# Kernel tuning notes

Measured on AMD Instinct MI355X. Metric: run time of the kernel, lower is better.

## Reference

```python
import jax, jax.numpy as jnp
import numpy as np

ROT_DIM = 32  # min(32, dim_head)

def rotate_half(t):
    # '... (j d) -> ... j d' with j=2, unbind, cat(-x2, x1)
    x1, x2 = jnp.split(t, 2, axis=-1)
    return jnp.concatenate((-x2, x1), axis=-1)

def apply_rotary(pos, t):
    rot_dim = pos.shape[-1]
    t_rot, t_pass = t[..., :rot_dim], t[..., rot_dim:]
    t_rot = t_rot * jnp.cos(pos) + rotate_half(t_rot) * jnp.sin(pos)
    return jnp.concatenate((t_rot, t_pass), axis=-1)

def setup_inputs() -> dict:
    key = jax.random.key(0)
    k1, k2, k3 = jax.random.split(key, 3)
    b, n, dim = 2, 2048, 2048
    inner = 16 * 128
    x = jax.random.normal(k1, (b, n, dim), dtype=jnp.float32)
    w_qkv = jax.random.normal(k2, (3 * inner, dim), dtype=jnp.float32) * (dim ** -0.5)
    w_out = jax.random.normal(k3, (inner, dim), dtype=jnp.float32) * (inner ** -0.5)
    g = jnp.ones((dim,), dtype=jnp.float32)
    return {"x": x, "w_qkv": w_qkv, "w_out": w_out, "g": g}

def reference(x, w_qkv, w_out, g):
    b, n, dim = x.shape
    h, d = 16, 128
    scale = d ** -0.5
    # NOTE: original code computes qkv from RAW x; the LayerNorm result is unused.
    qkv = jnp.einsum('bnc,fc->bnf', x, w_qkv)  # [b, n, 3*h*d]
    q, k, v = jnp.split(qkv, 3, axis=-1)
    def to_heads(t):  # b n (h d) -> (b h) n d
        return t.reshape(b, n, h, d).transpose(0, 2, 1, 3).reshape(b * h, n, d)
    q, k, v = map(to_heads, (q, k, v))
    # rotary positions: freqs [n, ROT_DIM//2], cat -> [n, ROT_DIM]
    inv_freq = 1.0 / (10000.0 ** (jnp.arange(0, ROT_DIM, 2, dtype=jnp.float32) / ROT_DIM))
    freqs = jnp.arange(n, dtype=jnp.float32)[:, None] * inv_freq[None, :]
    pos = jnp.concatenate((freqs, freqs), axis=-1)  # [n, ROT_DIM]
    q = apply_rotary(pos, q)
    k = apply_rotary(pos, k)
    q = q * scale
    sim = jnp.einsum('bid,bjd->bij', q, k)  # [(b h), n, n]
    causal_mask = jnp.triu(jnp.ones((n, n), dtype=bool), 1)
    neg = -jnp.finfo(sim.dtype).max
    sim = jnp.where(causal_mask[None], neg, sim)
    attn = jax.nn.softmax(sim, axis=-1)
    out = jnp.einsum('bij,bjd->bid', attn, v)  # [(b h), n, d]
    out = out.reshape(b, h, n, d).transpose(0, 2, 1, 3).reshape(b, n, h * d)
    return jnp.einsum('bnf,fc->bnc', out, w_out.T)  # Linear(inner, dim): y = out @ w_out^T with w_out [inner, dim]? see note
```

## Files before the change

### kernel.cpp

```cpp
#include <hip/hip_runtime.h>
#include <hip/hip_bf16.h>
#include <stdint.h>

typedef __bf16 bf16_t;
typedef __bf16 bf16x8 __attribute__((ext_vector_type(8)));
typedef float  f32x4  __attribute__((ext_vector_type(4)));

__device__ __forceinline__ void gload16(const void* gp, void* lp) {
  __builtin_amdgcn_global_load_lds(
      (const __attribute__((address_space(1))) void*)(uintptr_t)gp,
      (__attribute__((address_space(3))) void*)(uintptr_t)lp,
      16, 0, 0);
}

__device__ __forceinline__ f32x4 mfma16(bf16x8 a, bf16x8 b, f32x4 c) {
  return __builtin_amdgcn_mfma_f32_16x16x32_bf16(a, b, c, 0, 0, 0);
}

__device__ __forceinline__ uint32_t pack2(float a, float b) {
  uint16_t ba = __builtin_bit_cast(uint16_t, (bf16_t)a);
  uint16_t bb = __builtin_bit_cast(uint16_t, (bf16_t)b);
  return (uint32_t)ba | ((uint32_t)bb << 16);
}

__global__ __launch_bounds__(256) void cast_f32_to_bf16(const float* __restrict__ in,
                                                        bf16_t* __restrict__ out, int n8) {
  int i = blockIdx.x * 256 + threadIdx.x;
  int stride = gridDim.x * 256;
  for (; i < n8; i += stride) {
    const f32x4* p = (const f32x4*)in + (size_t)i * 2;
    f32x4 a = p[0], b = p[1];
    bf16x8 o;
    o[0] = (bf16_t)a[0]; o[1] = (bf16_t)a[1]; o[2] = (bf16_t)a[2]; o[3] = (bf16_t)a[3];
    o[4] = (bf16_t)b[0]; o[5] = (bf16_t)b[1]; o[6] = (bf16_t)b[2]; o[7] = (bf16_t)b[3];
    ((bf16x8*)out)[i] = o;
  }
}

template<bool OUT_BF16>
__global__ __launch_bounds__(512, 2) void gemm_bt_wide(const bf16_t* __restrict__ A,
                                                       const bf16_t* __restrict__ B,
                                                       void* __restrict__ Cout,
                                                       int M, int N, int K) {
  __shared__ __align__(16) bf16_t As[2][256 * 64];
  __shared__ __align__(16) bf16_t Bs[2][192 * 64];
  const int t = threadIdx.x;
  const int wid = t >> 6, l = t & 63;
  const int l15 = l & 15, l4 = l >> 4;
  const int wm = wid >> 1, wn = wid & 1;
  const long m0 = (long)blockIdx.x * 256;
  const long n0 = (long)blockIdx.y * 192;
  const int KT = K >> 6;

  auto stageA = [&](int kt, bf16_t* __restrict__ LB) {
    #pragma unroll
    for (int it = 0; it < 4; ++it) {
      int s = it * 512 + t;
      int r = s >> 3, c = s & 7;
      gload16(A + (m0 + r) * (long)K + kt * 64 + ((c ^ (r & 7)) << 3),
              LB + r * 64 + c * 8);
    }
  };
  auto stageB = [&](int kt, bf16_t* __restrict__ LB) {
    #pragma unroll
    for (int it = 0; it < 3; ++it) {
      int s = it * 512 + t;
      int r = s >> 3, c = s & 7;
      gload16(B + (n0 + r) * (long)K + kt * 64 + ((c ^ (r & 7)) << 3),
              LB + r * 64 + c * 8);
    }
  };
  auto ldfrag = [&](const bf16_t* buf, int rloc, int kk) -> bf16x8 {
    return *(const bf16x8*)(buf + rloc * 64 + ((((kk << 2) + l4) ^ (rloc & 7)) << 3));
  };

  f32x4 acc[4][6] = {};

  stageB(0, &Bs[0][0]);
  stageA(0, &As[0][0]);
  stageB(1, &Bs[1][0]);
  asm volatile("s_waitcnt vmcnt(3)" ::: "memory");
  asm volatile("s_barrier" ::: "memory");

  for (int kt = 0; kt < KT; ++kt) {
    const bf16_t* Ab = &As[kt & 1][0];
    const bf16_t* Bb = &Bs[kt & 1][0];
    const bool stA = (kt + 1 < KT), stB = (kt + 2 < KT);

    bf16x8 bfr[6][2];
    #pragma unroll
    for (int nr = 0; nr < 6; ++nr)
      #pragma unroll
      for (int kk = 0; kk < 2; ++kk)
        bfr[nr][kk] = ldfrag(Bb, wn * 96 + nr * 16 + l15, kk);
    {
      bf16x8 a0 = ldfrag(Ab, wm * 64 + 0 * 16 + l15, 0);
      bf16x8 a1 = ldfrag(Ab, wm * 64 + 1 * 16 + l15, 0);
      bf16x8 a2 = ldfrag(Ab, wm * 64 + 2 * 16 + l15, 0);
      bf16x8 a3 = ldfrag(Ab, wm * 64 + 3 * 16 + l15, 0);
      if (stA) stageA(kt + 1, &As[(kt + 1) & 1][0]);
      asm volatile("s_barrier" ::: "memory");
      asm volatile("s_waitcnt lgkmcnt(0)" ::: "memory");
      __builtin_amdgcn_sched_barrier(0);
      __builtin_amdgcn_s_setprio(1);
      #pragma unroll
      for (int nr = 0; nr < 6; ++nr) {
        acc[0][nr] = mfma16(a0, bfr[nr][0], acc[0][nr]);
        acc[1][nr] = mfma16(a1, bfr[nr][0], acc[1][nr]);
        acc[2][nr] = mfma16(a2, bfr[nr][0], acc[2][nr]);
        acc[3][nr] = mfma16(a3, bfr[nr][0], acc[3][nr]);
      }
      __builtin_amdgcn_s_setprio(0);
      asm volatile("s_barrier" ::: "memory");
    }
    {
      bf16x8 a0 = ldfrag(Ab, wm * 64 + 0 * 16 + l15, 1);
      bf16x8 a1 = ldfrag(Ab, wm * 64 + 1 * 16 + l15, 1);
      bf16x8 a2 = ldfrag(Ab, wm * 64 + 2 * 16 + l15, 1);
      bf16x8 a3 = ldfrag(Ab, wm * 64 + 3 * 16 + l15, 1);
      if (stB) stageB(kt + 2, &Bs[kt & 1][0]);
      asm volatile("s_barrier" ::: "memory");
      asm volatile("s_waitcnt lgkmcnt(0)" ::: "memory");
      __builtin_amdgcn_sched_barrier(0);
      __builtin_amdgcn_s_setprio(1);
      #pragma unroll
      for (int nr = 0; nr < 6; ++nr) {
        acc[0][nr] = mfma16(a0, bfr[nr][1], acc[0][nr]);
        acc[1][nr] = mfma16(a1, bfr[nr][1], acc[1][nr]);
        acc[2][nr] = mfma16(a2, bfr[nr][1], acc[2][nr]);
        acc[3][nr] = mfma16(a3, bfr[nr][1], acc[3][nr]);
      }
      __builtin_amdgcn_s_setprio(0);
      if (stB) asm volatile("s_waitcnt vmcnt(3)" ::: "memory");
      else     asm volatile("s_waitcnt vmcnt(0)" ::: "memory");
      asm volatile("s_barrier" ::: "memory");
    }
  }

  #pragma unroll
  for (int mr = 0; mr < 4; ++mr)
    #pragma unroll
    for (int nr = 0; nr < 6; ++nr)
      #pragma unroll
      for (int i = 0; i < 4; ++i) {
        long r = m0 + wm * 64 + mr * 16 + l4 * 4 + i;
        long c = n0 + wn * 96 + nr * 16 + l15;
        if (OUT_BF16) ((bf16_t*)Cout)[r * N + c] = (bf16_t)acc[mr][nr][i];
        else          ((float*)Cout)[r * N + c] = acc[mr][nr][i];
      }
}

template<bool OUT_BF16>
__global__ __launch_bounds__(512, 2) void gemm8p_bt(const bf16_t* __restrict__ A,
                                                    const bf16_t* __restrict__ B,
                                                    void* __restrict__ Cout,
                                                    int M, int N, int K) {
  __shared__ __align__(16) bf16_t As[2][128 * 64];
  __shared__ __align__(16) bf16_t Bs[2][256 * 64];
  const int t = threadIdx.x;
  const int wid = t >> 6, l = t & 63;
  const int l15 = l & 15, l4 = l >> 4;
  const int wm = wid >> 2, wn = wid & 3;
  const long m0 = (long)blockIdx.x * 128;
  const long n0 = (long)blockIdx.y * 256;
  const int KT = K >> 6;

  auto stageA = [&](int kt, bf16_t* __restrict__ LB) {
    #pragma unroll
    for (int it = 0; it < 2; ++it) {
      int s = it * 512 + t;
      int r = s >> 3, c = s & 7;
      gload16(A + (m0 + r) * (long)K + kt * 64 + ((c ^ (r & 7)) << 3),
              LB + r * 64 + c * 8);
    }
  };
  auto stageB = [&](int kt, bf16_t* __restrict__ LB) {
    #pragma unroll
    for (int it = 0; it < 4; ++it) {
      int s = it * 512 + t;
      int r = s >> 3, c = s & 7;
      gload16(B + (n0 + r) * (long)K + kt * 64 + ((c ^ (r & 7)) << 3),
              LB + r * 64 + c * 8);
    }
  };
  auto ldfrag = [&](const bf16_t* buf, int rloc, int kk) -> bf16x8 {
    return *(const bf16x8*)(buf + rloc * 64 + ((((kk << 2) + l4) ^ (rloc & 7)) << 3));
  };

  f32x4 acc[4][4] = {};

  stageB(0, &Bs[0][0]);
  stageA(0, &As[0][0]);
  stageB(1, &Bs[1][0]);
  asm volatile("s_waitcnt vmcnt(4)" ::: "memory");
  asm volatile("s_barrier" ::: "memory");

  for (int kt = 0; kt < KT; ++kt) {
    const bf16_t* Ab = &As[kt & 1][0];
    const bf16_t* Bb = &Bs[kt & 1][0];
    const bool stA = (kt + 1 < KT), stB = (kt + 2 < KT);

    bf16x8 bfr[4][2];
    #pragma unroll
    for (int nr = 0; nr < 4; ++nr)
      #pragma unroll
      for (int kk = 0; kk < 2; ++kk)
        bfr[nr][kk] = ldfrag(Bb, wn * 64 + nr * 16 + l15, kk);
    {
      bf16x8 a00 = ldfrag(Ab, wm * 64 + 0 * 16 + l15, 0);
      bf16x8 a01 = ldfrag(Ab, wm * 64 + 0 * 16 + l15, 1);
      bf16x8 a10 = ldfrag(Ab, wm * 64 + 1 * 16 + l15, 0);
      bf16x8 a11 = ldfrag(Ab, wm * 64 + 1 * 16 + l15, 1);
      if (stA) stageA(kt + 1, &As[(kt + 1) & 1][0]);
      asm volatile("s_barrier" ::: "memory");
      asm volatile("s_waitcnt lgkmcnt(0)" ::: "memory");
      __builtin_amdgcn_sched_barrier(0);
      __builtin_amdgcn_s_setprio(1);
      #pragma unroll
      for (int nr = 0; nr < 4; ++nr) {
        acc[0][nr] = mfma16(a00, bfr[nr][0], acc[0][nr]);
        acc[0][nr] = mfma16(a01, bfr[nr][1], acc[0][nr]);
        acc[1][nr] = mfma16(a10, bfr[nr][0], acc[1][nr]);
        acc[1][nr] = mfma16(a11, bfr[nr][1], acc[1][nr]);
      }
      __builtin_amdgcn_s_setprio(0);
      asm volatile("s_barrier" ::: "memory");
    }
    {
      bf16x8 a00 = ldfrag(Ab, wm * 64 + 2 * 16 + l15, 0);
      bf16x8 a01 = ldfrag(Ab, wm * 64 + 2 * 16 + l15, 1);
      bf16x8 a10 = ldfrag(Ab, wm * 64 + 3 * 16 + l15, 0);
      bf16x8 a11 = ldfrag(Ab, wm * 64 + 3 * 16 + l15, 1);
      if (stB) stageB(kt + 2, &Bs[kt & 1][0]);
      asm volatile("s_barrier" ::: "memory");
      asm volatile("s_waitcnt lgkmcnt(0)" ::: "memory");
      __builtin_amdgcn_sched_barrier(0);
      __builtin_amdgcn_s_setprio(1);
      #pragma unroll
      for (int nr = 0; nr < 4; ++nr) {
        acc[2][nr] = mfma16(a00, bfr[nr][0], acc[2][nr]);
        acc[2][nr] = mfma16(a01, bfr[nr][1], acc[2][nr]);
        acc[3][nr] = mfma16(a10, bfr[nr][0], acc[3][nr]);
        acc[3][nr] = mfma16(a11, bfr[nr][1], acc[3][nr]);
      }
      __builtin_amdgcn_s_setprio(0);
      if (stB) asm volatile("s_waitcnt vmcnt(4)" ::: "memory");
      else     asm volatile("s_waitcnt vmcnt(0)" ::: "memory");
      asm volatile("s_barrier" ::: "memory");
    }
  }

  #pragma unroll
  for (int mr = 0; mr < 4; ++mr)
    #pragma unroll
    for (int nr = 0; nr < 4; ++nr)
      #pragma unroll
      for (int i = 0; i < 4; ++i) {
        long r = m0 + wm * 64 + mr * 16 + l4 * 4 + i;
        long c = n0 + wn * 64 + nr * 16 + l15;
        if (OUT_BF16) ((bf16_t*)Cout)[r * N + c] = (bf16_t)acc[mr][nr][i];
        else          ((float*)Cout)[r * N + c] = acc[mr][nr][i];
      }
}

__global__ __launch_bounds__(256) void rope_scale(bf16_t* __restrict__ qkv) {
  int t = blockIdx.x * 256 + threadIdx.x;
  int m = t >> 8;
  int h = (t >> 4) & 15;
  int j = t & 15;
  int n = m & 2047;
  const float L2_10000_D16 = 0.8304820237218406f;
  float inv = exp2f(-(float)j * L2_10000_D16);
  float ang = (float)n * inv;
  float s, c;
  sincosf(ang, &s, &c);
  const float scale = 0.08838834764831845f;
  bf16_t* qp = qkv + (long)m * 6144 + h * 128;
  float a = (float)qp[j], b = (float)qp[j + 16];
  qp[j]      = (bf16_t)((a * c - b * s) * scale);
  qp[j + 16] = (bf16_t)((b * c + a * s) * scale);
  #pragma unroll
  for (int u = 0; u < 6; ++u) {
    int d = 32 + j + u * 16;
    qp[d] = (bf16_t)((float)qp[d] * scale);
  }
  bf16_t* kp = qp + 2048;
  a = (float)kp[j]; b = (float)kp[j + 16];
  kp[j]      = (bf16_t)(a * c - b * s);
  kp[j + 16] = (bf16_t)(b * c + a * s);
}

__global__ __launch_bounds__(512, 4) void attn_causal(const bf16_t* __restrict__ qkv,
                                                      bf16_t* __restrict__ ao) {
  const int id = blockIdx.x;
  const int qt = 15 - (id >> 5);
  const int bh = id & 31;
  const int b = bh >> 4, h = bh & 15;
  const int t = threadIdx.x;
  const int wid = t >> 6, l = t & 63;
  const int l15 = l & 15, l4 = l >> 4;
  __shared__ __align__(16) bf16_t Ks0[64 * 128];
  __shared__ __align__(16) bf16_t Ks1[64 * 128];
  __shared__ __align__(16) bf16_t Vt[128 * 64];
  __shared__ __align__(16) bf16_t Pb[8][16 * 72];
  const bf16_t* base = qkv + (long)b * 2048 * 6144 + h * 128;
  const int q0w = qt * 128 + wid * 16;
  bf16x8 qf[4];
  #pragma unroll
  for (int ks = 0; ks < 4; ++ks)
    qf[ks] = *(const bf16x8*)(base + (long)(q0w + l15) * 6144 + ks * 32 + l4 * 8);
  f32x4 o[8] = {};
  float mrun = -1.0e30f, lrun = 0.f;
  bf16_t* pbuf = Pb[wid];
  bf16x8 vr0, vr1;
  const int ntiles = 2 * qt + 2;

  auto stageK = [&](int tile, bf16_t* dst) {
    const bf16_t* src = base + 2048 + (long)tile * 64 * 6144;
    #pragma unroll
    for (int it = 0; it < 2; ++it) {
      int s = it * 512 + t;
      int krow = s >> 4, kc = s & 15;
      int ksc = kc ^ (krow & 7);
      gload16(src + (long)krow * 6144 + ksc * 8, dst + (size_t)s * 8);
    }
  };
  auto loadV = [&](int tile) {
    const bf16_t* vsr = base + 4096 + (long)(tile * 64 + l) * 6144;
    vr0 = *(const bf16x8*)(vsr + wid * 8);
    vr1 = *(const bf16x8*)(vsr + (8 + wid) * 8);
  };
  auto writeVt = [&]() {
    #pragma unroll
    for (int it = 0; it < 2; ++it) {
      int c = it * 8 + wid;
      bf16x8 v = it ? vr1 : vr0;
      #pragma unroll
      for (int e = 0; e < 8; ++e) {
        int d = c * 8 + e;
        Vt[d * 64 + (((l >> 3) ^ e) * 8) + (l & 7)] = v[e];
      }
    }
  };
  auto compute = [&](int kv0, const bf16_t* ksb) {
    if (kv0 > q0w + 15) return;
    f32x4 sa[4] = {};
    __builtin_amdgcn_s_setprio(1);
    #pragma unroll
    for (int ks = 0; ks < 4; ++ks) {
      #pragma unroll
      for (int nb = 0; nb < 4; ++nb) {
        int row = nb * 16 + l15;
        int cs = (ks * 4 + l4) ^ (row & 7);
        bf16x8 kf = *(const bf16x8*)(ksb + row * 128 + cs * 8);
        sa[nb] = mfma16(kf, qf[ks], sa[nb]);
      }
    }
    __builtin_amdgcn_s_setprio(0);
    if (kv0 + 63 > q0w) {
      const int q = q0w + l15;
      #pragma unroll
      for (int nb = 0; nb < 4; ++nb)
        #pragma unroll
        for (int i = 0; i < 4; ++i)
          if (kv0 + nb * 16 + l4 * 4 + i > q) sa[nb][i] = -3.0e38f;
    }
    f32x4 mv;
    #pragma unroll
    for (int i = 0; i < 4; ++i)
      mv[i] = fmaxf(fmaxf(sa[0][i], sa[1][i]), fmaxf(sa[2][i], sa[3][i]));
    float pmax = fmaxf(fmaxf(mv[0], mv[1]), fmaxf(mv[2], mv[3]));
    pmax = fmaxf(pmax, __shfl_xor(pmax, 16));
    pmax = fmaxf(pmax, __shfl_xor(pmax, 32));
    if (!__all(pmax - mrun <= 8.0f)) {
      float mnew = fmaxf(mrun, pmax);
      float corr = __expf(mrun - mnew);
      mrun = mnew;
      lrun *= corr;
      float cc[4];
      #pragma unroll
      for (int i = 0; i < 4; ++i) cc[i] = __shfl(corr, l4 * 4 + i);
      #pragma unroll
      for (int nf = 0; nf < 8; ++nf)
        #pragma unroll
        for (int i = 0; i < 4; ++i) o[nf][i] *= cc[i];
    }
    float ps = 0.f;
    #pragma unroll
    for (int nb = 0; nb < 4; ++nb)
      #pragma unroll
      for (int i = 0; i < 4; ++i) {
        float p = __expf(sa[nb][i] - mrun);
        sa[nb][i] = p;
        ps += p;
      }
    ps += __shfl_xor(ps, 16);
    ps += __shfl_xor(ps, 32);
    lrun += ps;
    #pragma unroll
    for (int nb = 0; nb < 4; ++nb) {
      int cw = (nb * 2 + (l4 >> 1)) ^ (l15 & 7);
      uint32_t* dst = (uint32_t*)(pbuf + l15 * 72 + cw * 8 + (l4 & 1) * 4);
      dst[0] = pack2(sa[nb][0], sa[nb][1]);
      dst[1] = pack2(sa[nb][2], sa[nb][3]);
    }
    #pragma unroll
    for (int ks2 = 0; ks2 < 2; ++ks2) {
      bf16x8 pf = *(const bf16x8*)(pbuf + l15 * 72 + (((ks2 * 4 + l4) ^ (l15 & 7)) * 8));
      __builtin_amdgcn_s_setprio(1);
      #pragma unroll
      for (int nf = 0; nf < 8; ++nf) {
        int row = nf * 16 + l15;
        bf16x8 vf = *(const bf16x8*)(Vt + row * 64 + (((ks2 * 4 + l4) ^ (row & 7)) * 8));
        o[nf] = mfma16(pf, vf, o[nf]);
      }
      __builtin_amdgcn_s_setprio(0);
    }
  };

  stageK(0, Ks0);
  loadV(0);
  writeVt();
  __syncthreads();
  for (int tile = 0; tile < ntiles; ++tile) {
    bf16_t* cur = (tile & 1) ? Ks1 : Ks0;
    bf16_t* nxt = (tile & 1) ? Ks0 : Ks1;
    const bool pre = (tile + 1 < ntiles);
    if (pre) { stageK(tile + 1, nxt); loadV(tile + 1); }
    compute(tile * 64, cur);
    __syncthreads();
    if (pre) writeVt();
    __syncthreads();
  }
  float linv = 1.f / lrun;
  float li[4];
  #pragma unroll
  for (int i = 0; i < 4; ++i) li[i] = __shfl(linv, l4 * 4 + i);
  bf16_t* aob = ao + (long)b * 2048 * 2048 + h * 128;
  #pragma unroll
  for (int i = 0; i < 4; ++i) {
    long qrow = q0w + l4 * 4 + i;
    #pragma unroll
    for (int nf = 0; nf < 8; ++nf)
      aob[qrow * 2048 + nf * 16 + l15] = (bf16_t)(o[nf][i] * li[i]);
  }
}

extern "C" void kernel_launch(void* const* d_in, const int* in_sizes, int n_in,
                              void* d_out, int out_size, void* d_ws, size_t ws_size,
                              hipStream_t stream) {
  const float* x     = (const float*)d_in[0];
  const float* w_qkv = (const float*)d_in[1];
  const float* w_out = (const float*)d_in[2];
  char* ws = (char*)d_ws;
  bf16_t* xb    = (bf16_t*)(ws + 0L);
  bf16_t* wqkvb = (bf16_t*)(ws + 16777216L);
  bf16_t* woutb = (bf16_t*)(ws + 41943040L);
  bf16_t* qkv   = (bf16_t*)(ws + 50331648L);
  bf16_t* ao    = (bf16_t*)(ws + 100663296L);

  cast_f32_to_bf16<<<2048, 256, 0, stream>>>(x, xb, 1048576);
  cast_f32_to_bf16<<<2048, 256, 0, stream>>>(w_qkv, wqkvb, 1572864);
  cast_f32_to_bf16<<<1024, 256, 0, stream>>>(w_out, woutb, 524288);
  gemm_bt_wide<true ><<<dim3(16, 32), 512, 0, stream>>>(xb, wqkvb, (void*)qkv, 4096, 6144, 2048);
  rope_scale<<<4096, 256, 0, stream>>>(qkv);
  attn_causal<<<512, 512, 0, stream>>>(qkv, ao);
  gemm8p_bt<false><<<dim3(32, 8), 512, 0, stream>>>(ao, woutb, d_out, 4096, 2048, 2048);
}
```

Before: 260.1 us.

## Widen QKV GEMM tile to 256x384 with K-step 32 and 8x6 accumulators

```diff
diff --git a/kernel.cpp b/kernel.cpp
--- a/kernel.cpp
+++ b/kernel.cpp
@@ -37,44 +37,41 @@
   }
 }
 
-template<bool OUT_BF16>
-__global__ __launch_bounds__(512, 2) void gemm_bt_wide(const bf16_t* __restrict__ A,
-                                                       const bf16_t* __restrict__ B,
-                                                       void* __restrict__ Cout,
-                                                       int M, int N, int K) {
-  __shared__ __align__(16) bf16_t As[2][256 * 64];
-  __shared__ __align__(16) bf16_t Bs[2][192 * 64];
+__global__ __launch_bounds__(512, 2) void gemm_qkv(const bf16_t* __restrict__ A,
+                                                   const bf16_t* __restrict__ B,
+                                                   bf16_t* __restrict__ C,
+                                                   int M, int N, int K) {
+  __shared__ __align__(16) bf16_t As[2][256 * 32];
+  __shared__ __align__(16) bf16_t Bs[2][384 * 32];
   const int t = threadIdx.x;
   const int wid = t >> 6, l = t & 63;
   const int l15 = l & 15, l4 = l >> 4;
-  const int wm = wid >> 1, wn = wid & 1;
+  const int wm = wid >> 2, wn = wid & 3;
   const long m0 = (long)blockIdx.x * 256;
-  const long n0 = (long)blockIdx.y * 192;
-  const int KT = K >> 6;
+  const long n0 = (long)blockIdx.y * 384;
+  const int KT = K >> 5;
 
   auto stageA = [&](int kt, bf16_t* __restrict__ LB) {
     #pragma unroll
-    for (int it = 0; it < 4; ++it) {
+    for (int it = 0; it < 2; ++it) {
       int s = it * 512 + t;
-      int r = s >> 3, c = s & 7;
-      gload16(A + (m0 + r) * (long)K + kt * 64 + ((c ^ (r & 7)) << 3),
-              LB + r * 64 + c * 8);
+      int r = s >> 2, c = s & 3;
+      gload16(A + (m0 + r) * (long)K + kt * 32 + c * 8, LB + r * 32 + c * 8);
     }
   };
   auto stageB = [&](int kt, bf16_t* __restrict__ LB) {
     #pragma unroll
     for (int it = 0; it < 3; ++it) {
       int s = it * 512 + t;
-      int r = s >> 3, c = s & 7;
-      gload16(B + (n0 + r) * (long)K + kt * 64 + ((c ^ (r & 7)) << 3),
-              LB + r * 64 + c * 8);
-    }
-  };
-  auto ldfrag = [&](const bf16_t* buf, int rloc, int kk) -> bf16x8 {
-    return *(const bf16x8*)(buf + rloc * 64 + ((((kk << 2) + l4) ^ (rloc & 7)) << 3));
-  };
-
-  f32x4 acc[4][6] = {};
+      int r = s >> 2, c = s & 3;
+      gload16(B + (n0 + r) * (long)K + kt * 32 + c * 8, LB + r * 32 + c * 8);
+    }
+  };
+  auto ldfrag = [&](const bf16_t* buf, int rloc) -> bf16x8 {
+    return *(const bf16x8*)(buf + rloc * 32 + l4 * 8);
+  };
+
+  f32x4 acc[8][6] = {};
 
   stageB(0, &Bs[0][0]);
   stageA(0, &As[0][0]);
@@ -87,17 +84,14 @@
     const bf16_t* Bb = &Bs[kt & 1][0];
     const bool stA = (kt + 1 < KT), stB = (kt + 2 < KT);
 
-    bf16x8 bfr[6][2];
-    #pragma unroll
-    for (int nr = 0; nr < 6; ++nr)
-      #pragma unroll
-      for (int kk = 0; kk < 2; ++kk)
-        bfr[nr][kk] = ldfrag(Bb, wn * 96 + nr * 16 + l15, kk);
+    bf16x8 bfr[6];
+    #pragma unroll
+    for (int nr = 0; nr < 6; ++nr) bfr[nr] = ldfrag(Bb, wn * 96 + nr * 16 + l15);
     {
-      bf16x8 a0 = ldfrag(Ab, wm * 64 + 0 * 16 + l15, 0);
-      bf16x8 a1 = ldfrag(Ab, wm * 64 + 1 * 16 + l15, 0);
-      bf16x8 a2 = ldfrag(Ab, wm * 64 + 2 * 16 + l15, 0);
-      bf16x8 a3 = ldfrag(Ab, wm * 64 + 3 * 16 + l15, 0);
+      bf16x8 a0 = ldfrag(Ab, wm * 128 + 0 * 16 + l15);
+      bf16x8 a1 = ldfrag(Ab, wm * 128 + 1 * 16 + l15);
+      bf16x8 a2 = ldfrag(Ab, wm * 128 + 2 * 16 + l15);
+      bf16x8 a3 = ldfrag(Ab, wm * 128 + 3 * 16 + l15);
       if (stA) stageA(kt + 1, &As[(kt + 1) & 1][0]);
       asm volatile("s_barrier" ::: "memory");
       asm volatile("s_waitcnt lgkmcnt(0)" ::: "memory");
@@ -105,19 +99,19 @@
       __builtin_amdgcn_s_setprio(1);
       #pragma unroll
       for (int nr = 0; nr < 6; ++nr) {
-        acc[0][nr] = mfma16(a0, bfr[nr][0], acc[0][nr]);
-        acc[1][nr] = mfma16(a1, bfr[nr][0], acc[1][nr]);
-        acc[2][nr] = mfma16(a2, bfr[nr][0], acc[2][nr]);
-        acc[3][nr] = mfma16(a3, bfr[nr][0], acc[3][nr]);
+        acc[0][nr] = mfma16(a0, bfr[nr], acc[0][nr]);
+        acc[1][nr] = mfma16(a1, bfr[nr], acc[1][nr]);
+        acc[2][nr] = mfma16(a2, bfr[nr], acc[2][nr]);
+        acc[3][nr] = mfma16(a3, bfr[nr], acc[3][nr]);
       }
       __builtin_amdgcn_s_setprio(0);
       asm volatile("s_barrier" ::: "memory");
     }
     {
-      bf16x8 a0 = ldfrag(Ab, wm * 64 + 0 * 16 + l15, 1);
-      bf16x8 a1 = ldfrag(Ab, wm * 64 + 1 * 16 + l15, 1);
-      bf16x8 a2 = ldfrag(Ab, wm * 64 + 2 * 16 + l15, 1);
-      bf16x8 a3 = ldfrag(Ab, wm * 64 + 3 * 16 + l15, 1);
+      bf16x8 a4 = ldfrag(Ab, wm * 128 + 4 * 16 + l15);
+      bf16x8 a5 = ldfrag(Ab, wm * 128 + 5 * 16 + l15);
+      bf16x8 a6 = ldfrag(Ab, wm * 128 + 6 * 16 + l15);
+      bf16x8 a7 = ldfrag(Ab, wm * 128 + 7 * 16 + l15);
       if (stB) stageB(kt + 2, &Bs[kt & 1][0]);
       asm volatile("s_barrier" ::: "memory");
       asm volatile("s_waitcnt lgkmcnt(0)" ::: "memory");
@@ -125,10 +119,10 @@
       __builtin_amdgcn_s_setprio(1);
       #pragma unroll
       for (int nr = 0; nr < 6; ++nr) {
-        acc[0][nr] = mfma16(a0, bfr[nr][1], acc[0][nr]);
-        acc[1][nr] = mfma16(a1, bfr[nr][1], acc[1][nr]);
-        acc[2][nr] = mfma16(a2, bfr[nr][1], acc[2][nr]);
-        acc[3][nr] = mfma16(a3, bfr[nr][1], acc[3][nr]);
+        acc[4][nr] = mfma16(a4, bfr[nr], acc[4][nr]);
+        acc[5][nr] = mfma16(a5, bfr[nr], acc[5][nr]);
+        acc[6][nr] = mfma16(a6, bfr[nr], acc[6][nr]);
+        acc[7][nr] = mfma16(a7, bfr[nr], acc[7][nr]);
       }
       __builtin_amdgcn_s_setprio(0);
       if (stB) asm volatile("s_waitcnt vmcnt(3)" ::: "memory");
@@ -138,15 +132,14 @@
   }
 
   #pragma unroll
-  for (int mr = 0; mr < 4; ++mr)
+  for (int mr = 0; mr < 8; ++mr)
     #pragma unroll
     for (int nr = 0; nr < 6; ++nr)
       #pragma unroll
       for (int i = 0; i < 4; ++i) {
-        long r = m0 + wm * 64 + mr * 16 + l4 * 4 + i;
+        long r = m0 + wm * 128 + mr * 16 + l4 * 4 + i;
         long c = n0 + wn * 96 + nr * 16 + l15;
-        if (OUT_BF16) ((bf16_t*)Cout)[r * N + c] = (bf16_t)acc[mr][nr][i];
-        else          ((float*)Cout)[r * N + c] = acc[mr][nr][i];
+        C[r * N + c] = (bf16_t)acc[mr][nr][i];
       }
 }
 
@@ -462,7 +455,7 @@
   cast_f32_to_bf16<<<2048, 256, 0, stream>>>(x, xb, 1048576);
   cast_f32_to_bf16<<<2048, 256, 0, stream>>>(w_qkv, wqkvb, 1572864);
   cast_f32_to_bf16<<<1024, 256, 0, stream>>>(w_out, woutb, 524288);
-  gemm_bt_wide<true ><<<dim3(16, 32), 512, 0, stream>>>(xb, wqkvb, (void*)qkv, 4096, 6144, 2048);
+  gemm_qkv<<<dim3(16, 16), 512, 0, stream>>>(xb, wqkvb, qkv, 4096, 6144, 2048);
   rope_scale<<<4096, 256, 0, stream>>>(qkv);
   attn_causal<<<512, 512, 0, stream>>>(qkv, ao);
   gemm8p_bt<false><<<dim3(32, 8), 512, 0, stream>>>(ao, woutb, d_out, 4096, 2048, 2048);
```

Measured after the change: 256.3 us. About the same (-1.5%).
